# Optimization experiments

Hardware: AMD Instinct MI355X
Metric: run time of the kernel (lower is better)

## Reference

```python
import jax, jax.numpy as jnp
import numpy as np

EPS = 1e-5
NUM_HEADS = 16
TEMP = 0.01

def _ln(x, g, b):
    m = jnp.mean(x, axis=-1, keepdims=True)
    v = jnp.var(x, axis=-1, keepdims=True)
    return (x - m) * jax.lax.rsqrt(v + EPS) * g + b

def setup_inputs() -> dict:
    key = jax.random.key(0)
    ks = jax.random.split(key, 16)
    b, l, c, ni = 4, 1024, 1024, 2
    d = c // NUM_HEADS
    s = lambda fan: 1.0 / np.sqrt(fan)
    return {
        "x_list": jax.random.normal(ks[0], (b, l, c, ni), jnp.float32),
        "w_": jax.random.normal(ks[1], (4 + ni, 1), jnp.float32),
        "qkv_w": jax.random.normal(ks[2], (3 * c, c), jnp.float32) * s(c),
        "qkv_b": jax.random.normal(ks[3], (3 * c,), jnp.float32) * 0.02,
        "proj_w": jax.random.normal(ks[4], (c, c), jnp.float32) * s(c),
        "proj_b": jax.random.normal(ks[5], (c,), jnp.float32) * 0.02,
        "nq_g": jnp.ones((d,), jnp.float32),
        "nq_b": jnp.zeros((d,), jnp.float32),
        "nk_g": jnp.ones((d,), jnp.float32),
        "nk_b": jnp.zeros((d,), jnp.float32),
        "conv_w": jax.random.normal(ks[6], (c, c), jnp.float32) * s(c),
        "conv_b": jax.random.normal(ks[7], (c,), jnp.float32) * 0.02,
        "ca1_w": jax.random.normal(ks[8], (c // 16, c), jnp.float32) * s(c),
        "ca1_b": jax.random.normal(ks[9], (c // 16,), jnp.float32) * 0.02,
        "ca2_w": jax.random.normal(ks[10], (c, c // 16), jnp.float32) * s(c // 16),
        "ca2_b": jax.random.normal(ks[11], (c,), jnp.float32) * 0.02,
        "mlp1_w": jax.random.normal(ks[12], (4 * c, c), jnp.float32) * s(c),
        "mlp1_b": jax.random.normal(ks[13], (4 * c,), jnp.float32) * 0.02,
        "mlp2_w": jax.random.normal(ks[14], (c, 4 * c), jnp.float32) * s(4 * c),
        "mlp2_b": jax.random.normal(ks[15], (c,), jnp.float32) * 0.02,
    }

def reference(x_list, w_, qkv_w, qkv_b, proj_w, proj_b, nq_g, nq_b, nk_g, nk_b,
              conv_w, conv_b, ca1_w, ca1_b, ca2_w, ca2_b, mlp1_w, mlp1_b, mlp2_w, mlp2_b):
    x = x_list[..., -1]  # [b, l, c]
    # op 0: Conv1x1Act = GELU(Linear)
    op0 = jax.nn.gelu(x @ conv_w.T + conv_b, approximate=False)
    # op 1: ChannelAttention = sigmoid(fc2(relu(fc1(x)))) * x
    op1 = jax.nn.sigmoid(jax.nn.relu(x @ ca1_w.T + ca1_b) @ ca2_w.T + ca2_b) * x
    # op 2: Identity
    op2 = x
    # op 3: MLP = fc2(GELU(fc1(x)))
    op3 = jax.nn.gelu(x @ mlp1_w.T + mlp1_b, approximate=False) @ mlp2_w.T + mlp2_b
    new = jnp.stack([op0, op1, op2, op3], axis=-1)  # [b, l, c, 4]
    xc = jnp.concatenate([x_list, new], axis=-1)    # [b, l, c, ni+4]
    w = jax.nn.softmax(w_ / TEMP, axis=0)           # [ni+4, 1]
    x = jnp.einsum('blcn,ni->blci', xc, w)[..., 0]  # [b, l, c]
    x_res = x
    # attention with per-head LayerNorm on q, k
    b_, n, c = x.shape
    d = c // NUM_HEADS
    qkv = x @ qkv_w.T + qkv_b
    q, k, v = jnp.split(qkv, 3, axis=-1)
    to_heads = lambda t: t.reshape(b_, n, NUM_HEADS, d).transpose(0, 2, 1, 3)  # [b, h, n, d]
    q, k, v = to_heads(q), to_heads(k), to_heads(v)
    q = _ln(q, nq_g, nq_b)
    k = _ln(k, nk_g, nk_b)
    score = jnp.einsum('bhnd,bhmd->bhnm', q, k) / np.sqrt(d).astype(np.float32)
    attn = jax.nn.softmax(score, axis=-1)           # [b, h, n, n]
    attn_map = attn.mean(axis=1)[:, 0, 1:]          # [b, n-1]
    out = jnp.einsum('bhnm,bhmd->bhnd', attn, v)
    out = out.transpose(0, 2, 1, 3).reshape(b_, n, c)
    out = out @ proj_w.T + proj_b + x_res
    return out, attn_map
```

## Files before the change

kernel.cpp:

```cpp
#include <hip/hip_runtime.h>
#include <hip/hip_bf16.h>

typedef __attribute__((ext_vector_type(8))) short short8;
typedef __attribute__((ext_vector_type(4))) float f32x4;

#define MROWS 4096
#define CDIM  1024
#define HEADS 16
#define DHEAD 64
#define NSEQ  1024

__device__ inline float softw(const float* __restrict__ w, int idx) {
    float m = w[0];
#pragma unroll
    for (int i = 1; i < 6; i++) m = fmaxf(m, w[i]);
    float s = 0.f, v = 0.f;
#pragma unroll
    for (int i = 0; i < 6; i++) {
        float e = __expf((w[i] - m) * 100.0f);
        s += e;
        if (i == idx) v = e;
    }
    return v / s;
}

__device__ inline float gelu_f(float x) {
    return 0.5f * x * (1.0f + erff(x * 0.70710678118654752f));
}

__global__ __launch_bounds__(256) void mix_base(
    const float* __restrict__ x_list, __hip_bfloat16* __restrict__ xb,
    float* __restrict__ am_acc)
{
    int i = blockIdx.x * 256 + threadIdx.x;
    xb[i] = __float2bfloat16(x_list[2 * (size_t)i + 1]);
    if (i < 4096) am_acc[i] = 0.f;
}

__global__ __launch_bounds__(256) void f2b(const float* __restrict__ in,
                                           __hip_bfloat16* __restrict__ out, int n)
{
    int i = blockIdx.x * 256 + threadIdx.x;
    if (i < n) out[i] = __float2bfloat16(in[i]);
}

#define BKT 32
#define LDA 40

template<int EPI, int FM, int FN>
__global__ __launch_bounds__(256) void gemm_bf16(
    const __hip_bfloat16* __restrict__ A, const __hip_bfloat16* __restrict__ W,
    const float* __restrict__ bias,
    float* __restrict__ f0, float* __restrict__ f1,
    __hip_bfloat16* __restrict__ b0, __hip_bfloat16* __restrict__ b1,
    __hip_bfloat16* __restrict__ b2,
    const float* __restrict__ g0, const float* __restrict__ be0,
    const float* __restrict__ g1, const float* __restrict__ be1,
    const float* __restrict__ wvec, int M, int N, int K)
{
    constexpr int BMt = FM * 32;
    constexpr int BNt = FN * 32;
    constexpr int NA = BMt / 64;
    constexpr int NB = BNt / 64;
    __shared__ __hip_bfloat16 As[2][BMt * LDA];
    __shared__ __hip_bfloat16 Bs[2][BNt * LDA];
    int t = threadIdx.x;
    int n0 = blockIdx.x * BNt, m0 = blockIdx.y * BMt;
    int wave = t >> 6, lane = t & 63;
    int wr = wave >> 1, wc = wave & 1;
    int quad = lane >> 4, l16 = lane & 15;
    int r0 = t >> 2, c0 = (t & 3) * 8;

    short8 sa0[NA], sb0[NB], sa1[NA], sb1[NB];
    auto ldg = [&](int k0, short8* da, short8* db) {
#pragma unroll
        for (int i = 0; i < NA; i++)
            da[i] = *(const short8*)(A + (size_t)(m0 + r0 + 64 * i) * K + k0 + c0);
#pragma unroll
        for (int i = 0; i < NB; i++)
            db[i] = *(const short8*)(W + (size_t)(n0 + r0 + 64 * i) * K + k0 + c0);
    };
    ldg(0, sa0, sb0);
    ldg(BKT, sa1, sb1);

    f32x4 zero = {0.f, 0.f, 0.f, 0.f};
    f32x4 acc[FM][FN];
#pragma unroll
    for (int i = 0; i < FM; i++)
#pragma unroll
        for (int j = 0; j < FN; j++) acc[i][j] = zero;

    for (int k0 = 0; k0 < K; k0 += 2 * BKT) {
#pragma unroll
        for (int i = 0; i < NA; i++)
            *(short8*)&As[0][(r0 + 64 * i) * LDA + c0] = sa0[i];
#pragma unroll
        for (int i = 0; i < NB; i++)
            *(short8*)&Bs[0][(r0 + 64 * i) * LDA + c0] = sb0[i];
        __syncthreads();
        if (k0 + 2 * BKT < K) ldg(k0 + 2 * BKT, sa0, sb0);
        {
            short8 af[FM], bf[FN];
#pragma unroll
            for (int i = 0; i < FM; i++)
                af[i] = *(const short8*)&As[0][(wr * FM * 16 + i * 16 + l16) * LDA + quad * 8];
#pragma unroll
            for (int j = 0; j < FN; j++)
                bf[j] = *(const short8*)&Bs[0][(wc * FN * 16 + j * 16 + l16) * LDA + quad * 8];
#pragma unroll
            for (int i = 0; i < FM; i++)
#pragma unroll
                for (int j = 0; j < FN; j++)
                    acc[i][j] = __builtin_amdgcn_mfma_f32_16x16x32_bf16(
                        af[i], bf[j], acc[i][j], 0, 0, 0);
        }
#pragma unroll
        for (int i = 0; i < NA; i++)
            *(short8*)&As[1][(r0 + 64 * i) * LDA + c0] = sa1[i];
#pragma unroll
        for (int i = 0; i < NB; i++)
            *(short8*)&Bs[1][(r0 + 64 * i) * LDA + c0] = sb1[i];
        __syncthreads();
        if (k0 + 3 * BKT < K) ldg(k0 + 3 * BKT, sa1, sb1);
        {
            short8 af[FM], bf[FN];
#pragma unroll
            for (int i = 0; i < FM; i++)
                af[i] = *(const short8*)&As[1][(wr * FM * 16 + i * 16 + l16) * LDA + quad * 8];
#pragma unroll
            for (int j = 0; j < FN; j++)
                bf[j] = *(const short8*)&Bs[1][(wc * FN * 16 + j * 16 + l16) * LDA + quad * 8];
#pragma unroll
            for (int i = 0; i < FM; i++)
#pragma unroll
                for (int j = 0; j < FN; j++)
                    acc[i][j] = __builtin_amdgcn_mfma_f32_16x16x32_bf16(
                        af[i], bf[j], acc[i][j], 0, 0, 0);
        }
    }

    if constexpr (EPI == 5) {
        int colbase = n0 + wc * FN * 16;
        int portion = colbase >> 10;
        int hh = (colbase >> 6) & 15;
        float bv[FN];
#pragma unroll
        for (int j = 0; j < FN; j++) bv[j] = bias[colbase + j * 16 + l16];
        if (portion == 2) {
#pragma unroll
            for (int i = 0; i < FM; i++)
#pragma unroll
                for (int j = 0; j < FN; j++)
#pragma unroll
                    for (int r = 0; r < 4; r++) {
                        int row = m0 + wr * FM * 16 + i * 16 + quad * 4 + r;
                        int bb = row >> 10, nn = row & 1023;
                        int dd = j * 16 + l16;
                        b0[((size_t)(bb * 16 + hh) * DHEAD + dd) * NSEQ + nn] =
                            __float2bfloat16(acc[i][j][r] + bv[j]);
                    }
        } else {
            const float* g  = (portion == 0) ? g0 : g1;
            const float* be = (portion == 0) ? be0 : be1;
            __hip_bfloat16* dst = (portion == 0) ? b1 : b2;
            float gv[FN], bev[FN];
#pragma unroll
            for (int j = 0; j < FN; j++) {
                gv[j] = g[j * 16 + l16];
                bev[j] = be[j * 16 + l16];
            }
#pragma unroll
            for (int i = 0; i < FM; i++)
#pragma unroll
                for (int r = 0; r < 4; r++) {
                    float s1 = 0.f, s2 = 0.f;
#pragma unroll
                    for (int j = 0; j < FN; j++) {
                        float v = acc[i][j][r] + bv[j];
                        s1 += v; s2 += v * v;
                    }
#pragma unroll
                    for (int mk = 1; mk < 16; mk <<= 1) {
                        s1 += __shfl_xor(s1, mk, 64);
                        s2 += __shfl_xor(s2, mk, 64);
                    }
                    float mean = s1 * (1.f / 64.f);
                    float var = s2 * (1.f / 64.f) - mean * mean;
                    float rs = rsqrtf(var + 1e-5f);
                    int row = m0 + wr * FM * 16 + i * 16 + quad * 4 + r;
                    int bb = row >> 10, nn = row & 1023;
                    size_t base = ((size_t)(bb * 16 + hh) * NSEQ + nn) * DHEAD;
#pragma unroll
                    for (int j = 0; j < FN; j++)
                        dst[base + j * 16 + l16] = __float2bfloat16(
                            (acc[i][j][r] + bv[j] - mean) * rs * gv[j] + bev[j]);
                }
        }
        return;
    }

    float wmx = 0.f, w0c = 0.f, w14c = 0.f;
    if (EPI == 1) {
        wmx = softw(wvec, 2);
        w0c = softw(wvec, 0);
        w14c = softw(wvec, 1) + softw(wvec, 4);
    }
    if (EPI == 3) wmx = softw(wvec, 5);

#pragma unroll
    for (int i = 0; i < FM; i++) {
#pragma unroll
        for (int j = 0; j < FN; j++) {
            int col = n0 + wc * FN * 16 + j * 16 + l16;
            float bv = bias[col];
#pragma unroll
            for (int r = 0; r < 4; r++) {
                int row = m0 + wr * FM * 16 + i * 16 + quad * 4 + r;
                float v = acc[i][j][r] + bv;
                size_t idx = (size_t)row * N + col;
                if (EPI == 1) {
                    float2 xl = *((const float2*)f1 + idx);
                    f0[idx] = w0c * xl.x + w14c * xl.y + wmx * gelu_f(v);
                } else if (EPI == 2) {
                    b0[idx] = __float2bfloat16(gelu_f(v));
                } else if (EPI == 3) {
                    float tv = f0[idx] + wmx * v;
                    f0[idx] = tv;
                    b0[idx] = __float2bfloat16(tv);
                } else if (EPI == 4) {
                    f0[idx] = v + f1[idx];
                }
            }
        }
    }
}

__global__ __launch_bounds__(256) void ca1_kernel(
    const __hip_bfloat16* __restrict__ xb, const float* __restrict__ w,
    const float* __restrict__ bias, float* __restrict__ h1)
{
    __shared__ float Xs[16 * 65];
    __shared__ float Ws[64 * 65];
    int t = threadIdx.x;
    int m0 = blockIdx.x * 16;
    int row = t >> 4, cg = t & 15;
    float acc[4] = {0.f, 0.f, 0.f, 0.f};
    for (int k0 = 0; k0 < 1024; k0 += 64) {
#pragma unroll
        for (int i = 0; i < 4; i++) {
            int e = t + i * 256; int r = e >> 6, c = e & 63;
            Xs[r * 65 + c] = __bfloat162float(xb[(size_t)(m0 + r) * 1024 + k0 + c]);
        }
#pragma unroll
        for (int i = 0; i < 16; i++) {
            int e = t + i * 256; int r = e >> 6, c = e & 63;
            Ws[r * 65 + c] = w[(size_t)r * 1024 + k0 + c];
        }
        __syncthreads();
        for (int k = 0; k < 64; k++) {
            float xv = Xs[row * 65 + k];
#pragma unroll
            for (int c = 0; c < 4; c++)
                acc[c] += xv * Ws[(cg * 4 + c) * 65 + k];
        }
        __syncthreads();
    }
#pragma unroll
    for (int c = 0; c < 4; c++)
        h1[(size_t)(m0 + row) * 64 + cg * 4 + c] =
            fmaxf(acc[c] + bias[cg * 4 + c], 0.f);
}

__global__ __launch_bounds__(256) void ca2_kernel(
    const float* __restrict__ h1, const float* __restrict__ w,
    const float* __restrict__ bias, const __hip_bfloat16* __restrict__ xb,
    float* __restrict__ xmix, const float* __restrict__ wvec)
{
    __shared__ float Wt[256 * 65];
    __shared__ float hs[16 * 64];
    int t = threadIdx.x;
    int m0 = blockIdx.x * 16, n0 = blockIdx.y * 256;
#pragma unroll
    for (int i = 0; i < 64; i++) {
        int e = t + i * 256; int r = e >> 6, c = e & 63;
        Wt[r * 65 + c] = w[(size_t)(n0 + r) * 64 + c];
    }
#pragma unroll
    for (int i = 0; i < 4; i++) {
        int e = t + i * 256; int r = e >> 6, c = e & 63;
        hs[r * 64 + c] = h1[(size_t)(m0 + r) * 64 + c];
    }
    __syncthreads();
    int n = n0 + t;
    float bv = bias[n];
    float acc[16];
#pragma unroll
    for (int mi = 0; mi < 16; mi++) acc[mi] = bv;
    for (int k = 0; k < 64; k++) {
        float wv = Wt[t * 65 + k];
#pragma unroll
        for (int mi = 0; mi < 16; mi++) acc[mi] += hs[mi * 64 + k] * wv;
    }
    float w3 = softw(wvec, 3);
#pragma unroll
    for (int mi = 0; mi < 16; mi++) {
        size_t idx = (size_t)(m0 + mi) * 1024 + n;
        float sg = 1.f / (1.f + __expf(-acc[mi]));
        xmix[idx] += w3 * sg * __bfloat162float(xb[idx]);
    }
}

#define PSTR 72
__global__ __launch_bounds__(256) void flash_mfma(
    const __hip_bfloat16* __restrict__ qb, const __hip_bfloat16* __restrict__ kb,
    const __hip_bfloat16* __restrict__ vt, __hip_bfloat16* __restrict__ ao)
{
    __shared__ __hip_bfloat16 Plds[4][32 * PSTR];
    int bh = blockIdx.x;
    int i0 = blockIdx.y * 128;
    int b = bh >> 4, h = bh & 15;
    int t = threadIdx.x, wave = t >> 6, lane = t & 63;
    int l16 = lane & 15, quad = lane >> 4;
    const __hip_bfloat16* qbase = qb + (size_t)bh * NSEQ * DHEAD;
    const __hip_bfloat16* kbase = kb + (size_t)bh * NSEQ * DHEAD;
    const __hip_bfloat16* vbase = vt + (size_t)bh * DHEAD * NSEQ;
    __hip_bfloat16* pw = Plds[wave];
    int qrow0 = i0 + wave * 32;

    short8 aq[2][2];
#pragma unroll
    for (int ri = 0; ri < 2; ri++)
#pragma unroll
        for (int ks = 0; ks < 2; ks++)
            aq[ri][ks] = *(const short8*)(qbase +
                (size_t)(qrow0 + ri * 16 + l16) * DHEAD + ks * 32 + quad * 8);

    f32x4 zero = {0.f, 0.f, 0.f, 0.f};
    f32x4 o[2][4];
    float mrow[2][4], lrow[2][4];
#pragma unroll
    for (int ri = 0; ri < 2; ri++) {
#pragma unroll
        for (int nt = 0; nt < 4; nt++) o[ri][nt] = zero;
#pragma unroll
        for (int rr = 0; rr < 4; rr++) { mrow[ri][rr] = -1e30f; lrow[ri][rr] = 0.f; }
    }

    for (int j0 = 0; j0 < NSEQ; j0 += 64) {
        short8 bk[4][2];
#pragma unroll
        for (int jt = 0; jt < 4; jt++)
#pragma unroll
            for (int ks = 0; ks < 2; ks++)
                bk[jt][ks] = *(const short8*)(kbase +
                    (size_t)(j0 + jt * 16 + l16) * DHEAD + ks * 32 + quad * 8);
        short8 bv[4][2];
#pragma unroll
        for (int nt = 0; nt < 4; nt++)
#pragma unroll
            for (int ks = 0; ks < 2; ks++)
                bv[nt][ks] = *(const short8*)(vbase +
                    (size_t)(nt * 16 + l16) * NSEQ + j0 + ks * 32 + quad * 8);

#pragma unroll
        for (int ri = 0; ri < 2; ri++) {
            f32x4 s[4];
#pragma unroll
            for (int jt = 0; jt < 4; jt++) s[jt] = zero;
#pragma unroll
            for (int jt = 0; jt < 4; jt++)
#pragma unroll
                for (int ks = 0; ks < 2; ks++)
                    s[jt] = __builtin_amdgcn_mfma_f32_16x16x32_bf16(
                        aq[ri][ks], bk[jt][ks], s[jt], 0, 0, 0);
#pragma unroll
            for (int rr = 0; rr < 4; rr++) {
                float mx = -1e30f;
#pragma unroll
                for (int jt = 0; jt < 4; jt++) {
                    s[jt][rr] *= 0.125f;
                    mx = fmaxf(mx, s[jt][rr]);
                }
#pragma unroll
                for (int mk = 1; mk < 16; mk <<= 1) mx = fmaxf(mx, __shfl_xor(mx, mk, 64));
                float om = mrow[ri][rr];
                float nm = fmaxf(om, mx);
                float al = __expf(om - nm);
                mrow[ri][rr] = nm;
                float ss = 0.f;
#pragma unroll
                for (int jt = 0; jt < 4; jt++) {
                    float p = __expf(s[jt][rr] - nm);
                    pw[(ri * 16 + quad * 4 + rr) * PSTR + jt * 16 + l16] =
                        __float2bfloat16(p);
                    ss += p;
                }
#pragma unroll
                for (int mk = 1; mk < 16; mk <<= 1) ss += __shfl_xor(ss, mk, 64);
                lrow[ri][rr] = lrow[ri][rr] * al + ss;
#pragma unroll
                for (int nt = 0; nt < 4; nt++) o[ri][nt][rr] *= al;
            }
        }
#pragma unroll
        for (int ri = 0; ri < 2; ri++) {
            short8 ap[2];
#pragma unroll
            for (int ks = 0; ks < 2; ks++)
                ap[ks] = *(const short8*)&pw[(ri * 16 + l16) * PSTR + ks * 32 + quad * 8];
#pragma unroll
            for (int nt = 0; nt < 4; nt++)
#pragma unroll
                for (int ks = 0; ks < 2; ks++)
                    o[ri][nt] = __builtin_amdgcn_mfma_f32_16x16x32_bf16(
                        ap[ks], bv[nt][ks], o[ri][nt], 0, 0, 0);
        }
    }

#pragma unroll
    for (int ri = 0; ri < 2; ri++)
#pragma unroll
        for (int rr = 0; rr < 4; rr++) {
            float inv = 1.f / lrow[ri][rr];
            int row = qrow0 + ri * 16 + quad * 4 + rr;
#pragma unroll
            for (int nt = 0; nt < 4; nt++)
                ao[((size_t)b * NSEQ + row) * CDIM + h * 64 + nt * 16 + l16] =
                    __float2bfloat16(o[ri][nt][rr] * inv);
        }
}

__global__ __launch_bounds__(256) void attn_map_acc(
    const __hip_bfloat16* __restrict__ qf, const __hip_bfloat16* __restrict__ kf,
    float* __restrict__ am)
{
    __shared__ float q0[64];
    __shared__ float red[256];
    int bh = blockIdx.x, t = threadIdx.x;
    const __hip_bfloat16* qr = qf + (size_t)bh * NSEQ * DHEAD;
    const __hip_bfloat16* kb = kf + (size_t)bh * NSEQ * DHEAD;
    if (t < 64) q0[t] = __bfloat162float(qr[t]);
    __syncthreads();
    float s[4];
    float mx = -1e30f;
#pragma unroll
    for (int ji = 0; ji < 4; ji++) {
        int j = ji * 256 + t;
        float a = 0.f;
        for (int k = 0; k < 64; k++) a += q0[k] * __bfloat162float(kb[(size_t)j * 64 + k]);
        a *= 0.125f;
        s[ji] = a;
        mx = fmaxf(mx, a);
    }
    red[t] = mx; __syncthreads();
    for (int st = 128; st > 0; st >>= 1) {
        if (t < st) red[t] = fmaxf(red[t], red[t + st]);
        __syncthreads();
    }
    float M = red[0]; __syncthreads();
    float sum = 0.f;
#pragma unroll
    for (int ji = 0; ji < 4; ji++) { s[ji] = __expf(s[ji] - M); sum += s[ji]; }
    red[t] = sum; __syncthreads();
    for (int st = 128; st > 0; st >>= 1) {
        if (t < st) red[t] += red[t + st];
        __syncthreads();
    }
    float inv = 1.f / red[0];
    int b = bh >> 4;
#pragma unroll
    for (int ji = 0; ji < 4; ji++) {
        int j = ji * 256 + t;
        if (j > 0) atomicAdd(&am[b * 1024 + j], s[ji] * inv * (1.f / 16.f));
    }
}

__global__ __launch_bounds__(256) void attn_map_out(
    const float* __restrict__ am, float* __restrict__ out1)
{
    int i = blockIdx.x * 256 + threadIdx.x;
    if (i < 4 * 1023) {
        int b = i / 1023;
        int j = i - b * 1023 + 1;
        out1[i] = am[b * 1024 + j];
    }
}

extern "C" void kernel_launch(void* const* d_in, const int* in_sizes, int n_in,
                              void* d_out, int out_size, void* d_ws, size_t ws_size,
                              hipStream_t stream)
{
    const float* x_list = (const float*)d_in[0];
    const float* wvec   = (const float*)d_in[1];
    const float* qkv_w  = (const float*)d_in[2];
    const float* qkv_b  = (const float*)d_in[3];
    const float* proj_w = (const float*)d_in[4];
    const float* proj_b = (const float*)d_in[5];
    const float* nq_g   = (const float*)d_in[6];
    const float* nq_b   = (const float*)d_in[7];
    const float* nk_g   = (const float*)d_in[8];
    const float* nk_b   = (const float*)d_in[9];
    const float* conv_w = (const float*)d_in[10];
    const float* conv_b = (const float*)d_in[11];
    const float* ca1_w  = (const float*)d_in[12];
    const float* ca1_b  = (const float*)d_in[13];
    const float* ca2_w  = (const float*)d_in[14];
    const float* ca2_b  = (const float*)d_in[15];
    const float* mlp1_w = (const float*)d_in[16];
    const float* mlp1_b = (const float*)d_in[17];
    const float* mlp2_w = (const float*)d_in[18];
    const float* mlp2_b = (const float*)d_in[19];

    float* out0 = (float*)d_out;
    float* out1 = out0 + (size_t)4 * 1024 * 1024;

    char* ws = (char*)d_ws;
    size_t off = 0;
    auto alloc = [&](size_t bytes) -> char* {
        char* p = ws + off;
        off += (bytes + 255) & ~(size_t)255;
        return p;
    };
    __hip_bfloat16* xb     = (__hip_bfloat16*)alloc((size_t)MROWS * CDIM * 2);
    float*          xmix   = (float*)alloc((size_t)MROWS * CDIM * 4);
    __hip_bfloat16* xmixb  = (__hip_bfloat16*)alloc((size_t)MROWS * CDIM * 2);
    float*          h1     = (float*)alloc((size_t)MROWS * 64 * 4);
    __hip_bfloat16* hb     = (__hip_bfloat16*)alloc((size_t)MROWS * 4096 * 2);
    __hip_bfloat16* qbb    = (__hip_bfloat16*)alloc((size_t)MROWS * CDIM * 2);
    __hip_bfloat16* kbb    = (__hip_bfloat16*)alloc((size_t)MROWS * CDIM * 2);
    __hip_bfloat16* vtb    = (__hip_bfloat16*)alloc((size_t)MROWS * CDIM * 2);
    __hip_bfloat16* aob    = (__hip_bfloat16*)alloc((size_t)MROWS * CDIM * 2);
    float*          amacc  = (float*)alloc(4096 * 4);
    __hip_bfloat16* convwb = (__hip_bfloat16*)alloc((size_t)1048576 * 2);
    __hip_bfloat16* qkvwb  = (__hip_bfloat16*)alloc((size_t)3145728 * 2);
    __hip_bfloat16* projwb = (__hip_bfloat16*)alloc((size_t)1048576 * 2);
    __hip_bfloat16* mlp1wb = (__hip_bfloat16*)alloc((size_t)4194304 * 2);
    __hip_bfloat16* mlp2wb = (__hip_bfloat16*)alloc((size_t)4194304 * 2);

    f2b<<<4096, 256, 0, stream>>>(conv_w, convwb, 1048576);
    f2b<<<12288, 256, 0, stream>>>(qkv_w, qkvwb, 3145728);
    f2b<<<4096, 256, 0, stream>>>(proj_w, projwb, 1048576);
    f2b<<<16384, 256, 0, stream>>>(mlp1_w, mlp1wb, 4194304);
    f2b<<<16384, 256, 0, stream>>>(mlp2_w, mlp2wb, 4194304);

    mix_base<<<16384, 256, 0, stream>>>(x_list, xb, amacc);

    gemm_bf16<1, 4, 2><<<dim3(16, 32), 256, 0, stream>>>(
        xb, convwb, conv_b, xmix, (float*)x_list, nullptr, nullptr, nullptr,
        nullptr, nullptr, nullptr, nullptr, wvec, MROWS, 1024, 1024);

    ca1_kernel<<<256, 256, 0, stream>>>(xb, ca1_w, ca1_b, h1);
    ca2_kernel<<<dim3(256, 4), 256, 0, stream>>>(h1, ca2_w, ca2_b, xb, xmix, wvec);

    gemm_bf16<2, 4, 4><<<dim3(32, 32), 256, 0, stream>>>(
        xb, mlp1wb, mlp1_b, nullptr, nullptr, hb, nullptr, nullptr,
        nullptr, nullptr, nullptr, nullptr, wvec, MROWS, 4096, 1024);
    gemm_bf16<3, 4, 2><<<dim3(16, 32), 256, 0, stream>>>(
        hb, mlp2wb, mlp2_b, xmix, nullptr, xmixb, nullptr, nullptr,
        nullptr, nullptr, nullptr, nullptr, wvec, MROWS, 1024, 4096);

    gemm_bf16<5, 4, 4><<<dim3(24, 32), 256, 0, stream>>>(
        xmixb, qkvwb, qkv_b, nullptr, nullptr, vtb, qbb, kbb,
        nq_g, nq_b, nk_g, nk_b, wvec, MROWS, 3072, 1024);

    flash_mfma<<<dim3(64, 8), 256, 0, stream>>>(qbb, kbb, vtb, aob);

    attn_map_acc<<<64, 256, 0, stream>>>(qbb, kbb, amacc);
    attn_map_out<<<16, 256, 0, stream>>>(amacc, out1);

    gemm_bf16<4, 4, 2><<<dim3(16, 32), 256, 0, stream>>>(
        aob, projwb, proj_b, out0, xmix, nullptr, nullptr, nullptr,
        nullptr, nullptr, nullptr, nullptr, wvec, MROWS, 1024, 1024);
}
```

Measured before the change: 548.8 us.

## Fuse conv and MLP1 GEMMs, keep mixed activation in bf16 only

Concatenates the conv and mlp1 weights so a single GEMM over N=5120 produces both the GELU conv mix and the MLP hidden activations, with a per-column epilogue branch. The fp32 xmix buffer is removed and the running mixed activation is kept only in bf16, which cuts memory traffic in the ca2, mlp2 and proj epilogues. The mlp2 and proj GEMMs also move to wider 4x4 tiles. Accumulating the mix and the residual in bf16 loses precision compared with fp32.

New measurement: 548.4 us. No clear change (-0.1%).

```diff
diff --git a/kernel.cpp b/kernel.cpp
--- a/kernel.cpp
+++ b/kernel.cpp
@@ -51,7 +51,7 @@
 __global__ __launch_bounds__(256) void gemm_bf16(
     const __hip_bfloat16* __restrict__ A, const __hip_bfloat16* __restrict__ W,
     const float* __restrict__ bias,
-    float* __restrict__ f0, float* __restrict__ f1,
+    float* __restrict__ f0, const float* __restrict__ f1,
     __hip_bfloat16* __restrict__ b0, __hip_bfloat16* __restrict__ b1,
     __hip_bfloat16* __restrict__ b2,
     const float* __restrict__ g0, const float* __restrict__ be0,
@@ -139,6 +139,37 @@
         }
     }
 
+    if constexpr (EPI == 1) {
+        float wmx = softw(wvec, 2);
+        float w0c = softw(wvec, 0);
+        float w14c = softw(wvec, 1) + softw(wvec, 4);
+        int colbase = n0 + wc * FN * 16;
+        bool isconv = colbase < 1024;
+#pragma unroll
+        for (int i = 0; i < FM; i++) {
+#pragma unroll
+            for (int j = 0; j < FN; j++) {
+                int col = colbase + j * 16 + l16;
+                float bv = isconv ? bias[col] : be0[col - 1024];
+#pragma unroll
+                for (int r = 0; r < 4; r++) {
+                    int row = m0 + wr * FM * 16 + i * 16 + quad * 4 + r;
+                    float v = acc[i][j][r] + bv;
+                    if (isconv) {
+                        size_t idx = (size_t)row * 1024 + col;
+                        float2 xl = ((const float2*)f1)[idx];
+                        b0[idx] = __float2bfloat16(
+                            w0c * xl.x + w14c * xl.y + wmx * gelu_f(v));
+                    } else {
+                        b1[(size_t)row * 4096 + (col - 1024)] =
+                            __float2bfloat16(gelu_f(v));
+                    }
+                }
+            }
+        }
+        return;
+    }
+
     if constexpr (EPI == 5) {
         int colbase = n0 + wc * FN * 16;
         int portion = colbase >> 10;
@@ -199,12 +230,7 @@
         return;
     }
 
-    float wmx = 0.f, w0c = 0.f, w14c = 0.f;
-    if (EPI == 1) {
-        wmx = softw(wvec, 2);
-        w0c = softw(wvec, 0);
-        w14c = softw(wvec, 1) + softw(wvec, 4);
-    }
+    float wmx = 0.f;
     if (EPI == 3) wmx = softw(wvec, 5);
 
 #pragma unroll
@@ -218,17 +244,11 @@
                 int row = m0 + wr * FM * 16 + i * 16 + quad * 4 + r;
                 float v = acc[i][j][r] + bv;
                 size_t idx = (size_t)row * N + col;
-                if (EPI == 1) {
-                    float2 xl = *((const float2*)f1 + idx);
-                    f0[idx] = w0c * xl.x + w14c * xl.y + wmx * gelu_f(v);
-                } else if (EPI == 2) {
-                    b0[idx] = __float2bfloat16(gelu_f(v));
-                } else if (EPI == 3) {
-                    float tv = f0[idx] + wmx * v;
-                    f0[idx] = tv;
+                if (EPI == 3) {
+                    float tv = __bfloat162float(b0[idx]) + wmx * v;
                     b0[idx] = __float2bfloat16(tv);
                 } else if (EPI == 4) {
-                    f0[idx] = v + f1[idx];
+                    f0[idx] = v + __bfloat162float(b1[idx]);
                 }
             }
         }
@@ -274,7 +294,7 @@
 __global__ __launch_bounds__(256) void ca2_kernel(
     const float* __restrict__ h1, const float* __restrict__ w,
     const float* __restrict__ bias, const __hip_bfloat16* __restrict__ xb,
-    float* __restrict__ xmix, const float* __restrict__ wvec)
+    __hip_bfloat16* __restrict__ xmixb, const float* __restrict__ wvec)
 {
     __shared__ float Wt[256 * 65];
     __shared__ float hs[16 * 64];
@@ -306,7 +326,8 @@
     for (int mi = 0; mi < 16; mi++) {
         size_t idx = (size_t)(m0 + mi) * 1024 + n;
         float sg = 1.f / (1.f + __expf(-acc[mi]));
-        xmix[idx] += w3 * sg * __bfloat162float(xb[idx]);
+        float cur = __bfloat162float(xmixb[idx]);
+        xmixb[idx] = __float2bfloat16(cur + w3 * sg * __bfloat162float(xb[idx]));
     }
 }
 
@@ -522,7 +543,6 @@
         return p;
     };
     __hip_bfloat16* xb     = (__hip_bfloat16*)alloc((size_t)MROWS * CDIM * 2);
-    float*          xmix   = (float*)alloc((size_t)MROWS * CDIM * 4);
     __hip_bfloat16* xmixb  = (__hip_bfloat16*)alloc((size_t)MROWS * CDIM * 2);
     float*          h1     = (float*)alloc((size_t)MROWS * 64 * 4);
     __hip_bfloat16* hb     = (__hip_bfloat16*)alloc((size_t)MROWS * 4096 * 2);
@@ -531,32 +551,28 @@
     __hip_bfloat16* vtb    = (__hip_bfloat16*)alloc((size_t)MROWS * CDIM * 2);
     __hip_bfloat16* aob    = (__hip_bfloat16*)alloc((size_t)MROWS * CDIM * 2);
     float*          amacc  = (float*)alloc(4096 * 4);
-    __hip_bfloat16* convwb = (__hip_bfloat16*)alloc((size_t)1048576 * 2);
+    __hip_bfloat16* wcat   = (__hip_bfloat16*)alloc((size_t)5120 * 1024 * 2);
     __hip_bfloat16* qkvwb  = (__hip_bfloat16*)alloc((size_t)3145728 * 2);
     __hip_bfloat16* projwb = (__hip_bfloat16*)alloc((size_t)1048576 * 2);
-    __hip_bfloat16* mlp1wb = (__hip_bfloat16*)alloc((size_t)4194304 * 2);
     __hip_bfloat16* mlp2wb = (__hip_bfloat16*)alloc((size_t)4194304 * 2);
 
-    f2b<<<4096, 256, 0, stream>>>(conv_w, convwb, 1048576);
+    f2b<<<4096, 256, 0, stream>>>(conv_w, wcat, 1048576);
+    f2b<<<16384, 256, 0, stream>>>(mlp1_w, wcat + (size_t)1048576, 4194304);
     f2b<<<12288, 256, 0, stream>>>(qkv_w, qkvwb, 3145728);
     f2b<<<4096, 256, 0, stream>>>(proj_w, projwb, 1048576);
-    f2b<<<16384, 256, 0, stream>>>(mlp1_w, mlp1wb, 4194304);
     f2b<<<16384, 256, 0, stream>>>(mlp2_w, mlp2wb, 4194304);
 
     mix_base<<<16384, 256, 0, stream>>>(x_list, xb, amacc);
 
-    gemm_bf16<1, 4, 2><<<dim3(16, 32), 256, 0, stream>>>(
-        xb, convwb, conv_b, xmix, (float*)x_list, nullptr, nullptr, nullptr,
-        nullptr, nullptr, nullptr, nullptr, wvec, MROWS, 1024, 1024);
+    gemm_bf16<1, 4, 4><<<dim3(40, 32), 256, 0, stream>>>(
+        xb, wcat, conv_b, nullptr, x_list, xmixb, hb, nullptr,
+        nullptr, mlp1_b, nullptr, nullptr, wvec, MROWS, 5120, 1024);
 
     ca1_kernel<<<256, 256, 0, stream>>>(xb, ca1_w, ca1_b, h1);
-    ca2_kernel<<<dim3(256, 4), 256, 0, stream>>>(h1, ca2_w, ca2_b, xb, xmix, wvec);
-
-    gemm_bf16<2, 4, 4><<<dim3(32, 32), 256, 0, stream>>>(
-        xb, mlp1wb, mlp1_b, nullptr, nullptr, hb, nullptr, nullptr,
-        nullptr, nullptr, nullptr, nullptr, wvec, MROWS, 4096, 1024);
-    gemm_bf16<3, 4, 2><<<dim3(16, 32), 256, 0, stream>>>(
-        hb, mlp2wb, mlp2_b, xmix, nullptr, xmixb, nullptr, nullptr,
+    ca2_kernel<<<dim3(256, 4), 256, 0, stream>>>(h1, ca2_w, ca2_b, xb, xmixb, wvec);
+
+    gemm_bf16<3, 4, 4><<<dim3(8, 32), 256, 0, stream>>>(
+        hb, mlp2wb, mlp2_b, nullptr, nullptr, xmixb, nullptr, nullptr,
         nullptr, nullptr, nullptr, nullptr, wvec, MROWS, 1024, 4096);
 
     gemm_bf16<5, 4, 4><<<dim3(24, 32), 256, 0, stream>>>(
@@ -568,7 +584,7 @@
     attn_map_acc<<<64, 256, 0, stream>>>(qbb, kbb, amacc);
     attn_map_out<<<16, 256, 0, stream>>>(amacc, out1);
 
-    gemm_bf16<4, 4, 2><<<dim3(16, 32), 256, 0, stream>>>(
-        aob, projwb, proj_b, out0, xmix, nullptr, nullptr, nullptr,
+    gemm_bf16<4, 4, 4><<<dim3(8, 32), 256, 0, stream>>>(
+        aob, projwb, proj_b, out0, nullptr, nullptr, xmixb, nullptr,
         nullptr, nullptr, nullptr, nullptr, wvec, MROWS, 1024, 1024);
 }
```
